# Kernel optimization log

Hardware: AMD Instinct MI355X
Metric: run time of the kernel (lower is better)

Reference implementation:

```python
import jax, jax.numpy as jnp
import numpy as np

HEADS = 4
DIM_HEAD = 32


def setup_inputs() -> dict:
    key = jax.random.key(0)
    k1, k2, k3, k4, k5 = jax.random.split(key, 5)
    dim = 128
    hidden = HEADS * DIM_HEAD  # 128
    h = w = 384
    x = jax.random.normal(k1, (1, dim, h, w), dtype=jnp.float32)
    # 1x1 conv weights (eqx Conv2d layout: [out_c, in_c, 1, 1]) + biases
    w_qkv = jax.random.normal(k2, (3 * hidden, dim, 1, 1), dtype=jnp.float32) * (1.0 / np.sqrt(dim))
    b_qkv = jax.random.normal(k3, (3 * hidden,), dtype=jnp.float32) * 0.01
    w_out = jax.random.normal(k4, (dim, hidden, 1, 1), dtype=jnp.float32) * (1.0 / np.sqrt(hidden))
    b_out = jax.random.normal(k5, (dim,), dtype=jnp.float32) * 0.01
    return {"x": x, "w_qkv": w_qkv, "b_qkv": b_qkv, "w_out": w_out, "b_out": b_out}


def reference(x, w_qkv, b_qkv, w_out, b_out):
    b, c, h, w = x.shape  # b == 1 (module squeezes batch)
    xs = x[0]  # (c, h, w)
    # 1x1 conv == channel matmul
    qkv = jnp.einsum('oc,chw->ohw', w_qkv[:, :, 0, 0], xs) + b_qkv[:, None, None]
    # rearrange '(qkv heads c) h w -> qkv heads c (h w)'
    qkv = qkv.reshape(3, HEADS, DIM_HEAD, h * w)
    q, k, v = qkv[0], qkv[1], qkv[2]  # each (heads, d, n)
    k = jax.nn.softmax(k, axis=-1)
    # context: (heads, d, e) -- small per-head outer product accumulated over n
    context = jnp.einsum('hdn,hen->hde', k, v)
    out = jnp.einsum('hde,hdn->hen', context, q)  # (heads, e, n)
    out = out.reshape(HEADS * DIM_HEAD, h, w)
    y = jnp.einsum('oc,chw->ohw', w_out[:, :, 0, 0], out) + b_out[:, None, None]
    return y  # (dim, h, w) -- module returns squeezed output
```

## Files before the change

kernel.cpp:

```cpp
#include <hip/hip_runtime.h>
#include <hip/hip_bf16.h>
#include <stdint.h>


#define NPOS 147456
#define NTILES 2304
#define NB1 512

typedef __attribute__((ext_vector_type(8))) short short8;
typedef __attribute__((ext_vector_type(4))) float floatx4;

__device__ __forceinline__ uint16_t f2bf(float f) {
    uint32_t u = __float_as_uint(f);
    return (uint16_t)((u + 0x7fffu + ((u >> 16) & 1u)) >> 16);
}
__device__ __forceinline__ uint32_t pack2(float a, float b) {
#if __has_builtin(__builtin_amdgcn_cvt_pk_bf16_f32)
    auto r = __builtin_amdgcn_cvt_pk_bf16_f32(a, b);
    uint32_t u; __builtin_memcpy(&u, &r, sizeof(u));
    return u;
#else
    return (uint32_t)f2bf(a) | ((uint32_t)f2bf(b) << 16);
#endif
}

#define XS_STRIDE 68
#define PS_STRIDE 36

__device__ __forceinline__ void k1_load(const float* __restrict__ xb, float* pf) {
    #pragma unroll
    for (int i = 0; i < 32; ++i) pf[i] = xb[(size_t)i * NPOS];
}
__device__ __forceinline__ void k1_store(uint32_t* Xsbuf, const float* pf, int lane, int c0) {
    #pragma unroll
    for (int i = 0; i < 8; ++i) {
        uint2 w;
        w.x = pack2(pf[i * 4 + 0], pf[i * 4 + 1]);
        w.y = pack2(pf[i * 4 + 2], pf[i * 4 + 3]);
        *(uint2*)&Xsbuf[lane * XS_STRIDE + (c0 + i * 4) / 2] = w;
    }
}
__device__ __forceinline__ void k1_tile(
    const uint32_t* __restrict__ Xsbuf, uint32_t* __restrict__ Psw,
    const short8 (&wfr)[4][4], const float (&biasv)[4],
    floatx4 (&acc2)[4], float (&sacc)[2], int m, int quad)
{
    #pragma unroll
    for (int nt = 0; nt < 4; ++nt) {
        short8 afr[4];
        #pragma unroll
        for (int ks = 0; ks < 4; ++ks)
            afr[ks] = *(const short8*)&Xsbuf[(nt * 16 + m) * XS_STRIDE + ks * 16 + quad * 4];
        floatx4 pa[4];
        #pragma unroll
        for (int kt = 0; kt < 4; ++kt) pa[kt] = (floatx4){0.f, 0.f, 0.f, 0.f};
        #pragma unroll
        for (int ks = 0; ks < 4; ++ks)
            #pragma unroll
            for (int kt = 0; kt < 4; ++kt)
                pa[kt] = __builtin_amdgcn_mfma_f32_16x16x32_bf16(afr[ks], wfr[kt][ks], pa[kt], 0, 0, 0);
        #pragma unroll
        for (int kt = 0; kt < 4; ++kt) {
            float v0 = pa[kt][0] + biasv[kt];
            float v1 = pa[kt][1] + biasv[kt];
            float v2 = pa[kt][2] + biasv[kt];
            float v3 = pa[kt][3] + biasv[kt];
            if (kt < 2) {
                v0 = __expf(v0); v1 = __expf(v1);
                v2 = __expf(v2); v3 = __expf(v3);
                sacc[kt] += (v0 + v1) + (v2 + v3);
            }
            uint2 w;
            w.x = pack2(v0, v1);
            w.y = pack2(v2, v3);
            *(uint2*)&Psw[(kt * 16 + m) * PS_STRIDE + nt * 8 + quad * 2] = w;
        }
    }
    #pragma unroll
    for (int ks = 0; ks < 2; ++ks) {
        short8 ea[2], vb[2];
        #pragma unroll
        for (int dt = 0; dt < 2; ++dt)
            ea[dt] = *(const short8*)&Psw[(dt * 16 + m) * PS_STRIDE + ks * 16 + quad * 4];
        #pragma unroll
        for (int et = 0; et < 2; ++et)
            vb[et] = *(const short8*)&Psw[(32 + et * 16 + m) * PS_STRIDE + ks * 16 + quad * 4];
        #pragma unroll
        for (int dt = 0; dt < 2; ++dt)
            #pragma unroll
            for (int et = 0; et < 2; ++et)
                acc2[dt * 2 + et] = __builtin_amdgcn_mfma_f32_16x16x32_bf16(ea[dt], vb[et], acc2[dt * 2 + et], 0, 0, 0);
    }
}

__global__ __launch_bounds__(256, 2) void k1_ctx(
    const float* __restrict__ x, const float* __restrict__ w_qkv,
    const float* __restrict__ b_qkv, float* __restrict__ cpart, int nb1)
{
    __shared__ uint32_t Xs[2][64 * XS_STRIDE];
    __shared__ uint32_t Ps[256 * PS_STRIDE];

    const int t = threadIdx.x;
    const int lane = t & 63;
    const int wavu = __builtin_amdgcn_readfirstlane(t >> 6);
    const int m = lane & 15, quad = lane >> 4;
    const int c0 = wavu * 32;
    uint32_t* const Psw = &Ps[wavu * 64 * PS_STRIDE];

    short8 wfr[4][4];
    float biasv[4];
    #pragma unroll
    for (int kt = 0; kt < 4; ++kt) {
        const int row = (kt < 2 ? 128 + wavu * 32 + kt * 16
                                : 256 + wavu * 32 + (kt - 2) * 16) + m;
        biasv[kt] = b_qkv[row];
        #pragma unroll
        for (int ks = 0; ks < 4; ++ks) {
            const float* p = w_qkv + row * 128 + ks * 32 + quad * 8;
            short8 w;
            #pragma unroll
            for (int j = 0; j < 8; ++j) w[j] = (short)f2bf(p[j]);
            wfr[kt][ks] = w;
        }
    }

    floatx4 acc2[4];
    #pragma unroll
    for (int i = 0; i < 4; ++i) acc2[i] = (floatx4){0.f, 0.f, 0.f, 0.f};
    float sacc[2] = {0.f, 0.f};

    const float* xw = x + (size_t)c0 * NPOS + lane;
    float pfA[32], pfB[32];

    k1_load(xw + blockIdx.x * 64, pfA);
    if (blockIdx.x + nb1 < NTILES) k1_load(xw + (blockIdx.x + nb1) * 64, pfB);
    k1_store(Xs[0], pfA, lane, c0);
    __syncthreads();

    for (int tile = blockIdx.x; tile < NTILES; tile += 2 * nb1) {
        const int t1 = tile + nb1, t2 = tile + 2 * nb1, t3 = tile + 3 * nb1;
        if (t2 < NTILES) k1_load(xw + t2 * 64, pfA);
        k1_tile(Xs[0], Psw, wfr, biasv, acc2, sacc, m, quad);
        if (t1 < NTILES) k1_store(Xs[1], pfB, lane, c0);
        __syncthreads();
        if (t1 < NTILES) {
            if (t3 < NTILES) k1_load(xw + t3 * 64, pfB);
            k1_tile(Xs[1], Psw, wfr, biasv, acc2, sacc, m, quad);
            if (t2 < NTILES) k1_store(Xs[0], pfA, lane, c0);
            __syncthreads();
        }
    }

    float* __restrict__ dst = cpart + (size_t)blockIdx.x * 4224;
    #pragma unroll
    for (int dt = 0; dt < 2; ++dt)
        #pragma unroll
        for (int et = 0; et < 2; ++et)
            #pragma unroll
            for (int r = 0; r < 4; ++r) {
                const int d = dt * 16 + quad * 4 + r, e = et * 16 + m;
                dst[wavu * 1024 + d * 32 + e] = acc2[dt * 2 + et][r];
            }
    #pragma unroll
    for (int kt = 0; kt < 2; ++kt) {
        float s = sacc[kt];
        s += __shfl_down(s, 32, 64);
        s += __shfl_down(s, 16, 64);
        if (lane < 16) dst[4096 + wavu * 32 + kt * 16 + lane] = s;
    }
}

__global__ void k2a(const float* __restrict__ cpart, float* __restrict__ ctxP, int nb1)
{
    const int u = blockIdx.x * 256 + threadIdx.x;
    if (u >= 4224 * 8) return;
    const int j = u % 4224, p = u / 4224;
    float s = 0.f;
    for (int b = p; b < nb1; b += 8) s += cpart[(size_t)b * 4224 + j];
    ctxP[p * 4224 + j] = s;
}

__global__ __launch_bounds__(128) void k2bc(
    const float* __restrict__ ctxP, const float* __restrict__ w_out,
    const float* __restrict__ w_qkv, const float* __restrict__ b_qkv,
    const float* __restrict__ b_out, uint32_t* __restrict__ Bmb, float* __restrict__ cvec)
{
    __shared__ float ctx33[128 * 33];
    __shared__ float Ss[128];
    __shared__ float Arow[128];
    __shared__ float row[128];
    __shared__ float red[128];
    const int o = blockIdx.x, t = threadIdx.x;
    for (int j = t; j < 4224; j += 128) {
        float s = 0.f;
        #pragma unroll
        for (int p = 0; p < 8; ++p) s += ctxP[p * 4224 + j];
        if (j < 4096) ctx33[(j >> 5) * 33 + (j & 31)] = s;
        else          Ss[j - 4096] = s;
    }
    __syncthreads();
    {
        const int h = t >> 5;
        float s = 0.f;
        #pragma unroll
        for (int e = 0; e < 32; ++e)
            s = fmaf(w_out[o * 128 + h * 32 + e], ctx33[t * 33 + e], s);
        Arow[t] = s / Ss[t];
    }
    __syncthreads();
    {
        float s = 0.f;
        #pragma unroll 16
        for (int hd = 0; hd < 128; ++hd)
            s = fmaf(Arow[hd], w_qkv[hd * 128 + t], s);
        row[t] = s;
    }
    red[t] = Arow[t] * b_qkv[t];
    __syncthreads();
    if (t < 64) Bmb[o * 64 + t] = pack2(row[2 * t], row[2 * t + 1]);
    if (t == 0) {
        float cs = b_out[o];
        #pragma unroll 8
        for (int i = 0; i < 128; ++i) cs += red[i];
        cvec[o] = cs;
    }
}

__global__ __launch_bounds__(256) void k3(
    const float* __restrict__ x, const uint32_t* __restrict__ Bmb,
    const float* __restrict__ cvec, float* __restrict__ y)
{
    __shared__ uint32_t Xs[64 * XS_STRIDE];
    const int t = threadIdx.x, lane = t & 63;
    const int wavu = __builtin_amdgcn_readfirstlane(t >> 6);
    const int m = lane & 15, quad = lane >> 4;
    const int n0 = blockIdx.x * 64;
    const int c0 = wavu * 32;

    float pf[32];
    k1_load(x + (size_t)c0 * NPOS + n0 + lane, pf);

    short8 bfr[2][4];
    float cv[2];
    #pragma unroll
    for (int ot = 0; ot < 2; ++ot) {
        const int o = (wavu * 2 + ot) * 16 + m;
        cv[ot] = cvec[o];
        #pragma unroll
        for (int ks = 0; ks < 4; ++ks)
            bfr[ot][ks] = *(const short8*)&Bmb[o * 64 + ks * 16 + quad * 4];
    }
    k1_store(Xs, pf, lane, c0);
    __syncthreads();

    floatx4 acc[2][4];
    #pragma unroll
    for (int ot = 0; ot < 2; ++ot)
        #pragma unroll
        for (int nt = 0; nt < 4; ++nt) acc[ot][nt] = (floatx4){0.f, 0.f, 0.f, 0.f};
    #pragma unroll
    for (int nt = 0; nt < 4; ++nt) {
        short8 afr[4];
        #pragma unroll
        for (int ks = 0; ks < 4; ++ks)
            afr[ks] = *(const short8*)&Xs[(nt * 16 + m) * XS_STRIDE + ks * 16 + quad * 4];
        #pragma unroll
        for (int ks = 0; ks < 4; ++ks)
            #pragma unroll
            for (int ot = 0; ot < 2; ++ot)
                acc[ot][nt] = __builtin_amdgcn_mfma_f32_16x16x32_bf16(afr[ks], bfr[ot][ks], acc[ot][nt], 0, 0, 0);
    }
    #pragma unroll
    for (int ot = 0; ot < 2; ++ot) {
        const int o = (wavu * 2 + ot) * 16 + m;
        #pragma unroll
        for (int nt = 0; nt < 4; ++nt) {
            floatx4 v = acc[ot][nt];
            v.x += cv[ot]; v.y += cv[ot]; v.z += cv[ot]; v.w += cv[ot];
            *(floatx4*)(y + (size_t)o * NPOS + n0 + nt * 16 + quad * 4) = v;
        }
    }
}

extern "C" void kernel_launch(void* const* d_in, const int* in_sizes, int n_in,
                              void* d_out, int out_size, void* d_ws, size_t ws_size,
                              hipStream_t stream)
{
    const float* x     = (const float*)d_in[0];
    const float* w_qkv = (const float*)d_in[1];
    const float* b_qkv = (const float*)d_in[2];
    const float* w_out = (const float*)d_in[3];
    const float* b_out = (const float*)d_in[4];
    float* y = (float*)d_out;

    const size_t tail = (size_t)(8 * 4224 + 8192 + 128) * 4;
    int nb1 = NB1;
    if (ws_size < tail + (size_t)nb1 * 16896) {
        long cap = ((long)ws_size - (long)tail) / 16896;
        nb1 = (int)cap;
        if (nb1 < 1) nb1 = 1;
        if (nb1 > NB1) nb1 = NB1;
    }
    char* wsb = (char*)d_ws;
    float* cpart   = (float*)wsb;
    float* ctxP    = (float*)(wsb + (size_t)nb1 * 16896);
    uint32_t* Bmb  = (uint32_t*)(ctxP + 8 * 4224);
    float* cvec    = (float*)(Bmb + 8192);

    hipLaunchKernelGGL(k1_ctx, dim3(nb1), dim3(256), 0, stream, x, w_qkv, b_qkv, cpart, nb1);
    hipLaunchKernelGGL(k2a, dim3(132), dim3(256), 0, stream, cpart, ctxP, nb1);
    hipLaunchKernelGGL(k2bc, dim3(128), dim3(128), 0, stream, ctxP, w_out, w_qkv, b_qkv, b_out, Bmb, cvec);
    hipLaunchKernelGGL(k3, dim3(NTILES), dim3(256), 0, stream, x, Bmb, cvec, y);
}
```

Baseline: 202.9 us.

## Replace partial-sum buffer and reduction kernel with atomic accumulation into 8 slots

Each k1 block now adds its context partials with float atomics into one of eight interleaved slots, instead of writing per-block partials that a separate k2a kernel reduced. This drops the k2a launch and the round trip of the cpart buffer, at the cost of a memset launch and atomic contention (64 blocks per slot). k2bc is widened to 256 threads for the slot reduction, with the later stages guarded to 128 threads. The workspace-size fallback logic is removed, so the code now assumes the workspace is large enough, and float atomic ordering makes results nondeterministic.

```diff
diff --git a/kernel.cpp b/kernel.cpp
--- a/kernel.cpp
+++ b/kernel.cpp
@@ -95,7 +95,7 @@
 
 __global__ __launch_bounds__(256, 2) void k1_ctx(
     const float* __restrict__ x, const float* __restrict__ w_qkv,
-    const float* __restrict__ b_qkv, float* __restrict__ cpart, int nb1)
+    const float* __restrict__ b_qkv, float* __restrict__ ctxP, int nb1)
 {
     __shared__ uint32_t Xs[2][64 * XS_STRIDE];
     __shared__ uint32_t Ps[256 * PS_STRIDE];
@@ -151,7 +151,7 @@
         }
     }
 
-    float* __restrict__ dst = cpart + (size_t)blockIdx.x * 4224;
+    float* __restrict__ dst = ctxP + (size_t)(blockIdx.x & 7) * 4224;
     #pragma unroll
     for (int dt = 0; dt < 2; ++dt)
         #pragma unroll
@@ -159,28 +159,18 @@
             #pragma unroll
             for (int r = 0; r < 4; ++r) {
                 const int d = dt * 16 + quad * 4 + r, e = et * 16 + m;
-                dst[wavu * 1024 + d * 32 + e] = acc2[dt * 2 + et][r];
+                atomicAdd(&dst[wavu * 1024 + d * 32 + e], acc2[dt * 2 + et][r]);
             }
     #pragma unroll
     for (int kt = 0; kt < 2; ++kt) {
         float s = sacc[kt];
         s += __shfl_down(s, 32, 64);
         s += __shfl_down(s, 16, 64);
-        if (lane < 16) dst[4096 + wavu * 32 + kt * 16 + lane] = s;
-    }
-}
-
-__global__ void k2a(const float* __restrict__ cpart, float* __restrict__ ctxP, int nb1)
-{
-    const int u = blockIdx.x * 256 + threadIdx.x;
-    if (u >= 4224 * 8) return;
-    const int j = u % 4224, p = u / 4224;
-    float s = 0.f;
-    for (int b = p; b < nb1; b += 8) s += cpart[(size_t)b * 4224 + j];
-    ctxP[p * 4224 + j] = s;
-}
-
-__global__ __launch_bounds__(128) void k2bc(
+        if (lane < 16) atomicAdd(&dst[4096 + wavu * 32 + kt * 16 + lane], s);
+    }
+}
+
+__global__ __launch_bounds__(256) void k2bc(
     const float* __restrict__ ctxP, const float* __restrict__ w_out,
     const float* __restrict__ w_qkv, const float* __restrict__ b_qkv,
     const float* __restrict__ b_out, uint32_t* __restrict__ Bmb, float* __restrict__ cvec)
@@ -191,7 +181,7 @@
     __shared__ float row[128];
     __shared__ float red[128];
     const int o = blockIdx.x, t = threadIdx.x;
-    for (int j = t; j < 4224; j += 128) {
+    for (int j = t; j < 4224; j += 256) {
         float s = 0.f;
         #pragma unroll
         for (int p = 0; p < 8; ++p) s += ctxP[p * 4224 + j];
@@ -199,7 +189,7 @@
         else          Ss[j - 4096] = s;
     }
     __syncthreads();
-    {
+    if (t < 128) {
         const int h = t >> 5;
         float s = 0.f;
         #pragma unroll
@@ -208,14 +198,14 @@
         Arow[t] = s / Ss[t];
     }
     __syncthreads();
-    {
+    if (t < 128) {
         float s = 0.f;
         #pragma unroll 16
         for (int hd = 0; hd < 128; ++hd)
             s = fmaf(Arow[hd], w_qkv[hd * 128 + t], s);
         row[t] = s;
-    }
-    red[t] = Arow[t] * b_qkv[t];
+        red[t] = Arow[t] * b_qkv[t];
+    }
     __syncthreads();
     if (t < 64) Bmb[o * 64 + t] = pack2(row[2 * t], row[2 * t + 1]);
     if (t == 0) {
@@ -293,22 +283,13 @@
     const float* b_out = (const float*)d_in[4];
     float* y = (float*)d_out;
 
-    const size_t tail = (size_t)(8 * 4224 + 8192 + 128) * 4;
-    int nb1 = NB1;
-    if (ws_size < tail + (size_t)nb1 * 16896) {
-        long cap = ((long)ws_size - (long)tail) / 16896;
-        nb1 = (int)cap;
-        if (nb1 < 1) nb1 = 1;
-        if (nb1 > NB1) nb1 = NB1;
-    }
     char* wsb = (char*)d_ws;
-    float* cpart   = (float*)wsb;
-    float* ctxP    = (float*)(wsb + (size_t)nb1 * 16896);
-    uint32_t* Bmb  = (uint32_t*)(ctxP + 8 * 4224);
-    float* cvec    = (float*)(Bmb + 8192);
-
-    hipLaunchKernelGGL(k1_ctx, dim3(nb1), dim3(256), 0, stream, x, w_qkv, b_qkv, cpart, nb1);
-    hipLaunchKernelGGL(k2a, dim3(132), dim3(256), 0, stream, cpart, ctxP, nb1);
-    hipLaunchKernelGGL(k2bc, dim3(128), dim3(128), 0, stream, ctxP, w_out, w_qkv, b_qkv, b_out, Bmb, cvec);
+    float* ctxP    = (float*)wsb;
+    uint32_t* Bmb  = (uint32_t*)(wsb + (size_t)8 * 4224 * 4);
+    float* cvec    = (float*)(wsb + (size_t)8 * 4224 * 4 + (size_t)8192 * 4);
+
+    hipMemsetAsync(ctxP, 0, (size_t)8 * 4224 * sizeof(float), stream);
+    hipLaunchKernelGGL(k1_ctx, dim3(NB1), dim3(256), 0, stream, x, w_qkv, b_qkv, ctxP, NB1);
+    hipLaunchKernelGGL(k2bc, dim3(128), dim3(256), 0, stream, ctxP, w_out, w_qkv, b_qkv, b_out, Bmb, cvec);
     hipLaunchKernelGGL(k3, dim3(NTILES), dim3(256), 0, stream, x, Bmb, cvec, y);
 }
```

Result: faster. 184.4 us (-9.1%).

## Stage k1 weights through LDS, use contiguous tile ranges, widen k2bc block

Applied to the files above, without the earlier changes.

In k1_ctx, qkv weight rows are now loaded coalesced into shared memory and converted to bf16 fragments from there, replacing per-lane strided global reads. The first x tile is prefetched before this weight setup so the two overlap. Each block now handles a contiguous range of tiles instead of a strided set. k2bc runs with 256 threads so its partial-context reduction loads go faster. The cost is extra barriers and LDS reuse during setup.

```diff
diff --git a/kernel.cpp b/kernel.cpp
--- a/kernel.cpp
+++ b/kernel.cpp
@@ -26,6 +26,7 @@
 
 #define XS_STRIDE 68
 #define PS_STRIDE 36
+#define WST_STRIDE 132
 
 __device__ __forceinline__ void k1_load(const float* __restrict__ xb, float* pf) {
     #pragma unroll
@@ -97,8 +98,10 @@
     const float* __restrict__ x, const float* __restrict__ w_qkv,
     const float* __restrict__ b_qkv, float* __restrict__ cpart, int nb1)
 {
-    __shared__ uint32_t Xs[2][64 * XS_STRIDE];
-    __shared__ uint32_t Ps[256 * PS_STRIDE];
+    __shared__ uint32_t smem[2 * 64 * XS_STRIDE + 256 * PS_STRIDE];
+    uint32_t* const Xs0 = smem;
+    uint32_t* const Xs1 = smem + 64 * XS_STRIDE;
+    uint32_t* const Ps  = smem + 2 * 64 * XS_STRIDE;
 
     const int t = threadIdx.x;
     const int lane = t & 63;
@@ -107,21 +110,47 @@
     const int c0 = wavu * 32;
     uint32_t* const Psw = &Ps[wavu * 64 * PS_STRIDE];
 
+    const int T0 = NTILES / nb1, R = NTILES % nb1;
+    const int b = blockIdx.x;
+    const int cnt = T0 + (b < R ? 1 : 0);
+    const int s0 = (b < R) ? b * (T0 + 1) : R * (T0 + 1) + (b - R) * T0;
+
+    const float* xw = x + (size_t)c0 * NPOS + lane;
+    float pfA[32], pfB[32];
+
+    k1_load(xw + (size_t)s0 * 64, pfA);
+
     short8 wfr[4][4];
     float biasv[4];
-    #pragma unroll
-    for (int kt = 0; kt < 4; ++kt) {
-        const int row = (kt < 2 ? 128 + wavu * 32 + kt * 16
-                                : 256 + wavu * 32 + (kt - 2) * 16) + m;
-        biasv[kt] = b_qkv[row];
-        #pragma unroll
-        for (int ks = 0; ks < 4; ++ks) {
-            const float* p = w_qkv + row * 128 + ks * 32 + quad * 8;
-            short8 w;
-            #pragma unroll
-            for (int j = 0; j < 8; ++j) w[j] = (short)f2bf(p[j]);
-            wfr[kt][ks] = w;
-        }
+    float* const Wst = (float*)smem + wavu * (32 * WST_STRIDE);
+    #pragma unroll
+    for (int pass = 0; pass < 2; ++pass) {
+        const int rbase = (pass == 0 ? 128 : 256) + wavu * 32;
+        const float* g = w_qkv + (size_t)rbase * 128;
+        #pragma unroll
+        for (int i = 0; i < 64; ++i) {
+            const int idx = i * 64 + lane;
+            Wst[(idx >> 7) * WST_STRIDE + (idx & 127)] = g[idx];
+        }
+        __syncthreads();
+        #pragma unroll
+        for (int kt = 0; kt < 2; ++kt) {
+            const int lr = kt * 16 + m;
+            #pragma unroll
+            for (int ks = 0; ks < 4; ++ks) {
+                const float* p = &Wst[lr * WST_STRIDE + ks * 32 + quad * 8];
+                float4 a = *(const float4*)p;
+                float4 c = *(const float4*)(p + 4);
+                short8 w;
+                w[0] = (short)f2bf(a.x); w[1] = (short)f2bf(a.y);
+                w[2] = (short)f2bf(a.z); w[3] = (short)f2bf(a.w);
+                w[4] = (short)f2bf(c.x); w[5] = (short)f2bf(c.y);
+                w[6] = (short)f2bf(c.z); w[7] = (short)f2bf(c.w);
+                wfr[pass * 2 + kt][ks] = w;
+            }
+            biasv[pass * 2 + kt] = b_qkv[rbase + kt * 16 + m];
+        }
+        __syncthreads();
     }
 
     floatx4 acc2[4];
@@ -129,24 +158,19 @@
     for (int i = 0; i < 4; ++i) acc2[i] = (floatx4){0.f, 0.f, 0.f, 0.f};
     float sacc[2] = {0.f, 0.f};
 
-    const float* xw = x + (size_t)c0 * NPOS + lane;
-    float pfA[32], pfB[32];
-
-    k1_load(xw + blockIdx.x * 64, pfA);
-    if (blockIdx.x + nb1 < NTILES) k1_load(xw + (blockIdx.x + nb1) * 64, pfB);
-    k1_store(Xs[0], pfA, lane, c0);
-    __syncthreads();
-
-    for (int tile = blockIdx.x; tile < NTILES; tile += 2 * nb1) {
-        const int t1 = tile + nb1, t2 = tile + 2 * nb1, t3 = tile + 3 * nb1;
-        if (t2 < NTILES) k1_load(xw + t2 * 64, pfA);
-        k1_tile(Xs[0], Psw, wfr, biasv, acc2, sacc, m, quad);
-        if (t1 < NTILES) k1_store(Xs[1], pfB, lane, c0);
+    if (cnt > 1) k1_load(xw + (size_t)(s0 + 1) * 64, pfB);
+    k1_store(Xs0, pfA, lane, c0);
+    __syncthreads();
+
+    for (int i = 0; i < cnt; i += 2) {
+        if (i + 2 < cnt) k1_load(xw + (size_t)(s0 + i + 2) * 64, pfA);
+        k1_tile(Xs0, Psw, wfr, biasv, acc2, sacc, m, quad);
+        if (i + 1 < cnt) k1_store(Xs1, pfB, lane, c0);
         __syncthreads();
-        if (t1 < NTILES) {
-            if (t3 < NTILES) k1_load(xw + t3 * 64, pfB);
-            k1_tile(Xs[1], Psw, wfr, biasv, acc2, sacc, m, quad);
-            if (t2 < NTILES) k1_store(Xs[0], pfA, lane, c0);
+        if (i + 1 < cnt) {
+            if (i + 3 < cnt) k1_load(xw + (size_t)(s0 + i + 3) * 64, pfB);
+            k1_tile(Xs1, Psw, wfr, biasv, acc2, sacc, m, quad);
+            if (i + 2 < cnt) k1_store(Xs0, pfA, lane, c0);
             __syncthreads();
         }
     }
@@ -180,7 +204,7 @@
     ctxP[p * 4224 + j] = s;
 }
 
-__global__ __launch_bounds__(128) void k2bc(
+__global__ __launch_bounds__(256) void k2bc(
     const float* __restrict__ ctxP, const float* __restrict__ w_out,
     const float* __restrict__ w_qkv, const float* __restrict__ b_qkv,
     const float* __restrict__ b_out, uint32_t* __restrict__ Bmb, float* __restrict__ cvec)
@@ -191,7 +215,7 @@
     __shared__ float row[128];
     __shared__ float red[128];
     const int o = blockIdx.x, t = threadIdx.x;
-    for (int j = t; j < 4224; j += 128) {
+    for (int j = t; j < 4224; j += 256) {
         float s = 0.f;
         #pragma unroll
         for (int p = 0; p < 8; ++p) s += ctxP[p * 4224 + j];
@@ -199,7 +223,7 @@
         else          Ss[j - 4096] = s;
     }
     __syncthreads();
-    {
+    if (t < 128) {
         const int h = t >> 5;
         float s = 0.f;
         #pragma unroll
@@ -208,14 +232,14 @@
         Arow[t] = s / Ss[t];
     }
     __syncthreads();
-    {
+    if (t < 128) {
         float s = 0.f;
         #pragma unroll 16
         for (int hd = 0; hd < 128; ++hd)
             s = fmaf(Arow[hd], w_qkv[hd * 128 + t], s);
         row[t] = s;
-    }
-    red[t] = Arow[t] * b_qkv[t];
+        red[t] = Arow[t] * b_qkv[t];
+    }
     __syncthreads();
     if (t < 64) Bmb[o * 64 + t] = pack2(row[2 * t], row[2 * t + 1]);
     if (t == 0) {
@@ -309,6 +333,6 @@
 
     hipLaunchKernelGGL(k1_ctx, dim3(nb1), dim3(256), 0, stream, x, w_qkv, b_qkv, cpart, nb1);
     hipLaunchKernelGGL(k2a, dim3(132), dim3(256), 0, stream, cpart, ctxP, nb1);
-    hipLaunchKernelGGL(k2bc, dim3(128), dim3(128), 0, stream, ctxP, w_out, w_qkv, b_qkv, b_out, Bmb, cvec);
+    hipLaunchKernelGGL(k2bc, dim3(128), dim3(256), 0, stream, ctxP, w_out, w_qkv, b_qkv, b_out, Bmb, cvec);
     hipLaunchKernelGGL(k3, dim3(NTILES), dim3(256), 0, stream, x, Bmb, cvec, y);
 }
```

After: 198.5 us. 1.02x faster.
